# Performance work log

Measured on AMD Instinct MI355X. Metric: run time of the kernel, lower is better.

The kernel has to match this reference:

```python
import jax, jax.numpy as jnp
import numpy as np

N_NODES = 150000
N_EDGES = 2400000


def setup_inputs() -> dict:
    key = jax.random.key(0)
    ks = jax.random.split(key, 7)
    x = jax.random.normal(ks[0], (N_NODES, 9), dtype=jnp.float32)
    edge_index = jax.random.randint(ks[1], (2, N_EDGES), 0, N_NODES, dtype=jnp.int32)
    edge_weight = jax.random.uniform(ks[2], (N_EDGES,), dtype=jnp.float32, minval=0.1, maxval=1.0)
    W1 = jax.random.normal(ks[3], (9, 32), dtype=jnp.float32) * (1.0 / np.sqrt(9))
    b1 = jnp.zeros((32,), dtype=jnp.float32)
    W2 = jax.random.normal(ks[4], (32, 7), dtype=jnp.float32) * (1.0 / np.sqrt(32))
    b2 = jnp.zeros((7,), dtype=jnp.float32)
    return {"x": x, "edge_index": edge_index, "edge_weight": edge_weight,
            "W1": W1, "b1": b1, "W2": W2, "b2": b2}


def gcn_norm(edge_index, edge_weight, num_nodes):
    # PyG gcn_norm: add self-loops (weight 1), symmetric D^-1/2 A D^-1/2
    row, col = edge_index[0], edge_index[1]
    loop = jnp.arange(num_nodes, dtype=edge_index.dtype)
    row = jnp.concatenate([row, loop])
    col = jnp.concatenate([col, loop])
    w = jnp.concatenate([edge_weight, jnp.ones((num_nodes,), edge_weight.dtype)])
    deg = jax.ops.segment_sum(w, col, num_segments=num_nodes)  # [N]
    dinv = jnp.where(deg > 0, jax.lax.rsqrt(deg), 0.0)
    norm = dinv[row] * w * dinv[col]  # [E+N]
    return row, col, norm


def gcn_conv(x, W, b, row, col, norm, num_nodes):
    h = x @ W                                   # [N, out]
    msg = norm[:, None] * h[row]                # [E+N, out] gather + scale
    out = jax.ops.segment_sum(msg, col, num_segments=num_nodes)  # scatter-add
    return out + b


def reference(x, edge_index, edge_weight, W1, b1, W2, b2):
    n = x.shape[0]
    row, col, norm = gcn_norm(edge_index, edge_weight, n)
    h = jax.nn.relu(gcn_conv(x, W1, b1, row, col, norm, n))
    # dropout is identity in eval mode
    h = gcn_conv(h, W2, b2, row, col, norm, n)
    return jax.nn.log_softmax(h, axis=1)
```

## Files before the change

kernel.cpp:

```cpp
#include <hip/hip_runtime.h>
#include <hip/hip_fp16.h>

constexpr int F_IN  = 9;
constexpr int F_HID = 32;
constexpr int F_OUT = 7;

constexpr int SB_SHIFT = 13;
constexpr int SB_NODES = 1 << SB_SHIFT;
constexpr int NSB      = 19;
constexpr int SB_CAP   = 135424;
constexpr int A_EDGES  = 4096;
constexpr int FB_PER_SB= SB_NODES / 256;
constexpr int NBKT     = 586;
constexpr int NBKT_PAD = NSB * FB_PER_SB;
constexpr int BCAP     = 4864;
constexpr int B_EDGES  = 4096;
constexpr int B_CHUNKS = (SB_CAP + B_EDGES - 1) / B_EDGES;
constexpr int ROW_MASK = (1 << 18) - 1;

__device__ __forceinline__ int nt_load_int(const int* p) {
    return __builtin_nontemporal_load(p);
}

__device__ __forceinline__ unsigned pack_h2(float a, float b) {
    return (unsigned)__half_as_ushort(__float2half(a)) |
           ((unsigned)__half_as_ushort(__float2half(b)) << 16);
}
__device__ __forceinline__ float2 unpack_h2(unsigned u) {
    return make_float2(__half2float(__ushort_as_half((unsigned short)(u & 0xffffu))),
                       __half2float(__ushort_as_half((unsigned short)(u >> 16))));
}

__global__ void k_zcur(int* __restrict__ bcur) {
    int i = blockIdx.x * 256 + threadIdx.x;
    if (i < NBKT_PAD) bcur[i * 16] = i * BCAP;
}

__global__ __launch_bounds__(256) void k_histA(
    const int* __restrict__ col, int* __restrict__ ghist, int nblkA, int E)
{
    __shared__ int h[NSB];
    const int tid = threadIdx.x;
    if (tid < NSB) h[tid] = 0;
    __syncthreads();
    const int t0 = blockIdx.x * A_EDGES;
    const int kend = min(A_EDGES, E - t0);
    for (int k = tid; k < kend; k += 256)
        atomicAdd(&h[col[t0 + k] >> SB_SHIFT], 1);
    __syncthreads();
    if (tid < NSB) ghist[(size_t)tid * nblkA + blockIdx.x] = h[tid];
}

__global__ __launch_bounds__(256) void k_scanA(
    int* __restrict__ ghist, int* __restrict__ sbcnt, int nblkA)
{
    __shared__ int sc[256];
    const int s = blockIdx.x, tid = threadIdx.x;
    int* r = ghist + (size_t)s * nblkA;
    const int per = (nblkA + 255) / 256;
    const int i0 = tid * per, i1 = min(i0 + per, nblkA);

    int sum = 0;
    for (int i = i0; i < i1; ++i) sum += r[i];
    sc[tid] = sum; __syncthreads();
    for (int d = 1; d < 256; d <<= 1) {
        int u = (tid >= d) ? sc[tid - d] : 0;
        __syncthreads();
        sc[tid] += u; __syncthreads();
    }
    int run = sc[tid] - sum;
    for (int i = i0; i < i1; ++i) { int v = r[i]; r[i] = run; run += v; }
    if (tid == 255) sbcnt[s] = run;
}

__global__ __launch_bounds__(256) void k_scatA(
    const int* __restrict__ row, const int* __restrict__ col,
    const float* __restrict__ w, const int* __restrict__ ghist,
    int2* __restrict__ sbrec, int nblkA, int E)
{
    __shared__ int rb[NSB];
    __shared__ int cur[NSB];
    const int b = blockIdx.x, tid = threadIdx.x;
    if (tid < NSB) {
        rb[tid] = tid * SB_CAP + ghist[(size_t)tid * nblkA + b];
        cur[tid] = 0;
    }
    __syncthreads();
    const int t0 = b * A_EDGES;
    const int kend = min(A_EDGES, E - t0);
    for (int k = tid; k < kend; k += 256) {
        int e = t0 + k;
        int c = col[e];
        int s = c >> SB_SHIFT;
        int2 rec = make_int2(row[e] | ((c & (SB_NODES - 1)) << 18),
                             __float_as_int(w[e]));
        int rk = atomicAdd(&cur[s], 1);
        int pos = rb[s] + rk;
        if (pos < (s + 1) * SB_CAP)
            sbrec[pos] = rec;
    }
}

__global__ __launch_bounds__(256) void k_fbkt(
    const int2* __restrict__ sbrec, const int* __restrict__ sbcnt,
    int* __restrict__ bcur, int2* __restrict__ irec)
{
    __shared__ int2 s_rec[B_EDGES];
    __shared__ int hist[FB_PER_SB * 4];
    __shared__ int rbase[FB_PER_SB * 4];

    const int sb    = blockIdx.x / B_CHUNKS;
    const int chunk = blockIdx.x % B_CHUNKS;
    const int cnt   = min(sbcnt[sb], SB_CAP);
    const int k0    = chunk * B_EDGES;
    const int kend  = min(B_EDGES, cnt - k0);
    if (kend <= 0) return;

    const int tid = threadIdx.x, wv = tid >> 6;
    for (int i = tid; i < FB_PER_SB * 4; i += 256) hist[i] = 0;
    __syncthreads();

    const int base = sb * SB_CAP + k0;
    for (int k = tid; k < kend; k += 256) {
        int2 rc = sbrec[base + k];
        s_rec[k] = rc;
        int fb = ((unsigned)rc.x >> 18) >> 8;
        atomicAdd(&hist[fb * 4 + wv], 1);
    }
    __syncthreads();
    for (int i = tid; i < FB_PER_SB * 4; i += 256) {
        int c = hist[i];
        int gb = sb * FB_PER_SB + (i >> 2);
        rbase[i] = c ? atomicAdd(&bcur[gb * 16], c) : 0;
        hist[i] = 0;
    }
    __syncthreads();
    for (int k = tid; k < kend; k += 256) {
        int2 rc = s_rec[k];
        int fb = ((unsigned)rc.x >> 18) >> 8;
        int idx = fb * 4 + wv;
        int rk = atomicAdd(&hist[idx], 1);
        int pos = rbase[idx] + rk;
        int gb = sb * FB_PER_SB + fb;
        if (pos < (gb + 1) * BCAP)
            irec[pos] = rc;
    }
}

__global__ __launch_bounds__(256) void k_sortbucket(
    int2* __restrict__ irec, int* __restrict__ csr4,
    const int* __restrict__ bcur, const float* __restrict__ x,
    int4* __restrict__ meta, unsigned* __restrict__ xdh, int N)
{
    __shared__ int2  s_rec[BCAP];
    __shared__ int   hist[256];
    __shared__ float wsum[256];
    __shared__ int   nbase[256];
    __shared__ int   scur[256];

    const int b    = blockIdx.x;
    const int tid  = threadIdx.x;
    const int base = b * BCAP;
    const int cnt  = min(bcur[b * 16] - base, BCAP);

    hist[tid] = 0; wsum[tid] = 0.0f; scur[tid] = 0;
    __syncthreads();

    for (int k = tid; k < cnt; k += 256) {
        int2 rc = irec[base + k];
        s_rec[k] = rc;
        int c = ((unsigned)rc.x >> 18) & 255;
        atomicAdd(&hist[c], 1);
        atomicAdd(&wsum[c], __int_as_float(rc.y));
    }
    __syncthreads();

    int v = hist[tid];
    nbase[tid] = v;
    __syncthreads();
    for (int d = 1; d < 256; d <<= 1) {
        int u = (tid >= d) ? nbase[tid - d] : 0;
        __syncthreads();
        nbase[tid] += u;
        __syncthreads();
    }
    int excl = nbase[tid] - v;
    __syncthreads();
    nbase[tid] = excl;

    int node = b * 256 + tid;
    float dv = rsqrtf(1.0f + wsum[tid]);
    if (node < N)
        meta[node] = make_int4(base + excl, v, __float_as_int(dv), 0);
    __syncthreads();

    if (node < N) {
        float xv[F_IN];
        #pragma unroll
        for (int j = 0; j < F_IN; ++j) xv[j] = dv * x[(size_t)node * F_IN + j];
        size_t o = (size_t)node * 6;
        xdh[o + 0] = pack_h2(xv[0], xv[1]);
        xdh[o + 1] = pack_h2(xv[2], xv[3]);
        xdh[o + 2] = pack_h2(xv[4], xv[5]);
        xdh[o + 3] = pack_h2(xv[6], xv[7]);
        xdh[o + 4] = pack_h2(xv[8], 0.0f);
        xdh[o + 5] = 0u;
    }

    for (int k = tid; k < cnt; k += 256) {
        int2 rc = s_rec[k];
        int c = ((unsigned)rc.x >> 18) & 255;
        int r = atomicAdd(&scur[c], 1);
        float wf = __int_as_float(rc.y);
        int wq = min((int)(wf * 16384.0f + 0.5f), 16383);
        csr4[base + nbase[c] + r] = ((rc.x & ROW_MASK) << 14) | wq;
    }
}

__global__ __launch_bounds__(256) void k_g1mlp(
    const int* __restrict__ csr4, const int4* __restrict__ meta,
    const unsigned* __restrict__ xdh,
    const float* __restrict__ W1, const float* __restrict__ b1,
    const float* __restrict__ W2, unsigned* __restrict__ h2dh, int N)
{
    __shared__ float sW1[F_IN * F_HID];
    __shared__ float sb1[F_HID];
    __shared__ float sW2[F_HID * F_OUT];
    for (int t = threadIdx.x; t < F_IN * F_HID; t += 256) sW1[t] = W1[t];
    for (int t = threadIdx.x; t < F_HID;        t += 256) sb1[t] = b1[t];
    for (int t = threadIdx.x; t < F_HID * F_OUT; t += 256) sW2[t] = W2[t];
    __syncthreads();

    int t   = blockIdx.x * 256 + threadIdx.x;
    int i   = t >> 2;
    int sub = t & 3;
    if (i >= N) return;
    int4 m = meta[i];
    float dv = __int_as_float(m.z);

    float acc[F_IN];
    #pragma unroll
    for (int j = 0; j < F_IN; ++j) acc[j] = 0.0f;
    if (sub == 0) {
        size_t o = (size_t)i * 6;
        uint2 u01 = *reinterpret_cast<const uint2*>(xdh + o);
        uint2 u23 = *reinterpret_cast<const uint2*>(xdh + o + 2);
        unsigned u4 = xdh[o + 4];
        float2 f0 = unpack_h2(u01.x), f1 = unpack_h2(u01.y),
               f2 = unpack_h2(u23.x), f3 = unpack_h2(u23.y),
               f4 = unpack_h2(u4);
        acc[0] = f0.x; acc[1] = f0.y; acc[2] = f1.x; acc[3] = f1.y;
        acc[4] = f2.x; acc[5] = f2.y; acc[6] = f3.x; acc[7] = f3.y;
        acc[8] = f4.x;
    }
    int s = m.x, tend = m.x + m.y;
    for (int e = s + sub; e < tend; e += 4) {
        int v = nt_load_int(&csr4[e]);
        int r = (int)((unsigned)v >> 14);
        float wv = (float)(v & 16383) * (1.0f / 16384.0f);
        size_t o = (size_t)r * 6;
        uint2 u01 = *reinterpret_cast<const uint2*>(xdh + o);
        uint2 u23 = *reinterpret_cast<const uint2*>(xdh + o + 2);
        unsigned u4 = xdh[o + 4];
        float2 f0 = unpack_h2(u01.x), f1 = unpack_h2(u01.y),
               f2 = unpack_h2(u23.x), f3 = unpack_h2(u23.y),
               f4 = unpack_h2(u4);
        acc[0] = fmaf(wv, f0.x, acc[0]); acc[1] = fmaf(wv, f0.y, acc[1]);
        acc[2] = fmaf(wv, f1.x, acc[2]); acc[3] = fmaf(wv, f1.y, acc[3]);
        acc[4] = fmaf(wv, f2.x, acc[4]); acc[5] = fmaf(wv, f2.y, acc[5]);
        acc[6] = fmaf(wv, f3.x, acc[6]); acc[7] = fmaf(wv, f3.y, acc[7]);
        acc[8] = fmaf(wv, f4.x, acc[8]);
    }
    #pragma unroll
    for (int d = 1; d < 4; d <<= 1) {
        #pragma unroll
        for (int j = 0; j < F_IN; ++j)
            acc[j] += __shfl_xor(acc[j], d, 4);
    }
    #pragma unroll
    for (int j = 0; j < F_IN; ++j) acc[j] *= dv;

    float o[F_OUT];
    #pragma unroll
    for (int c = 0; c < F_OUT; ++c) o[c] = 0.0f;
    int ks = sub * 8;
    #pragma unroll
    for (int k = 0; k < 8; ++k) {
        float hk = sb1[ks + k];
        #pragma unroll
        for (int j = 0; j < F_IN; ++j) hk = fmaf(acc[j], sW1[j * F_HID + ks + k], hk);
        hk = fmaxf(hk, 0.0f);
        #pragma unroll
        for (int c = 0; c < F_OUT; ++c) o[c] = fmaf(hk, sW2[(ks + k) * F_OUT + c], o[c]);
    }
    #pragma unroll
    for (int d = 1; d < 4; d <<= 1) {
        #pragma unroll
        for (int c = 0; c < F_OUT; ++c)
            o[c] += __shfl_xor(o[c], d, 4);
    }
    float pa = dv * o[2 * sub];
    float pb = (2 * sub + 1 < F_OUT) ? dv * o[2 * sub + 1] : 0.0f;
    h2dh[(size_t)i * 4 + sub] = pack_h2(pa, pb);
}

__global__ __launch_bounds__(256) void k_g2ls(
    const int* __restrict__ csr4, const int4* __restrict__ meta,
    const unsigned* __restrict__ h2dh, const float* __restrict__ b2,
    float* __restrict__ out, int N)
{
    int t   = blockIdx.x * 256 + threadIdx.x;
    int i   = t >> 2;
    int sub = t & 3;
    if (i >= N) return;
    int4 m = meta[i];
    float dv = __int_as_float(m.z);

    float acc[F_OUT];
    #pragma unroll
    for (int c = 0; c < F_OUT; ++c) acc[c] = 0.0f;
    if (sub == 0) {
        uint4 h4 = *reinterpret_cast<const uint4*>(h2dh + (size_t)i * 4);
        float2 f0 = unpack_h2(h4.x), f1 = unpack_h2(h4.y),
               f2 = unpack_h2(h4.z), f3 = unpack_h2(h4.w);
        acc[0] = f0.x; acc[1] = f0.y; acc[2] = f1.x; acc[3] = f1.y;
        acc[4] = f2.x; acc[5] = f2.y; acc[6] = f3.x;
    }
    int s = m.x, tend = m.x + m.y;
    for (int e = s + sub; e < tend; e += 4) {
        int v = nt_load_int(&csr4[e]);
        int r = (int)((unsigned)v >> 14);
        float wv = (float)(v & 16383) * (1.0f / 16384.0f);
        uint4 h4 = *reinterpret_cast<const uint4*>(h2dh + (size_t)r * 4);
        float2 f0 = unpack_h2(h4.x), f1 = unpack_h2(h4.y),
               f2 = unpack_h2(h4.z), f3 = unpack_h2(h4.w);
        acc[0] = fmaf(wv, f0.x, acc[0]); acc[1] = fmaf(wv, f0.y, acc[1]);
        acc[2] = fmaf(wv, f1.x, acc[2]); acc[3] = fmaf(wv, f1.y, acc[3]);
        acc[4] = fmaf(wv, f2.x, acc[4]); acc[5] = fmaf(wv, f2.y, acc[5]);
        acc[6] = fmaf(wv, f3.x, acc[6]);
    }
    #pragma unroll
    for (int d = 1; d < 4; d <<= 1) {
        #pragma unroll
        for (int c = 0; c < F_OUT; ++c)
            acc[c] += __shfl_xor(acc[c], d, 4);
    }

    float vv[F_OUT];
    float mx = -1e30f;
    #pragma unroll
    for (int c = 0; c < F_OUT; ++c) {
        vv[c] = dv * acc[c] + b2[c];
        mx = fmaxf(mx, vv[c]);
    }
    float ss = 0.0f;
    #pragma unroll
    for (int c = 0; c < F_OUT; ++c) ss += __expf(vv[c] - mx);
    float ls = __logf(ss);
    for (int c = sub; c < F_OUT; c += 4)
        out[(size_t)i * F_OUT + c] = vv[c] - mx - ls;
}

extern "C" void kernel_launch(void* const* d_in, const int* in_sizes, int n_in,
                              void* d_out, int out_size, void* d_ws, size_t ws_size,
                              hipStream_t stream) {
    const float* x  = (const float*)d_in[0];
    const int*   ei = (const int*)  d_in[1];
    const float* ew = (const float*)d_in[2];
    const float* W1 = (const float*)d_in[3];
    const float* b1 = (const float*)d_in[4];
    const float* W2 = (const float*)d_in[5];
    const float* b2 = (const float*)d_in[6];
    float* out = (float*)d_out;

    const int N = in_sizes[0] / F_IN;
    const int E = in_sizes[2];
    const int* row = ei;
    const int* col = ei + E;
    const int nblkA = (E + A_EDGES - 1) / A_EDGES;

    int2* sbrec = (int2*)d_ws;
    int2* irec  = sbrec + (size_t)NSB * SB_CAP;
    int*  csr4  = (int*)irec;
    int*  bcur  = (int*)(irec + (size_t)NBKT * BCAP);
    int*  ghist = bcur + (size_t)NBKT_PAD * 16;
    int*  sbcnt = ghist + (size_t)NSB * nblkA;
    int4*     meta = (int4*)d_ws;
    unsigned* xdh  = (unsigned*)(meta + N);
    unsigned* h2dh = xdh + (size_t)N * 6;

    const int gB = NSB * B_CHUNKS;
    const int gN4 = (4 * N + 255) / 256;

    k_zcur      <<<(NBKT_PAD + 255) / 256, 256, 0, stream>>>(bcur);
    k_histA     <<<nblkA, 256, 0, stream>>>(col, ghist, nblkA, E);
    k_scanA     <<<NSB, 256, 0, stream>>>(ghist, sbcnt, nblkA);
    k_scatA     <<<nblkA, 256, 0, stream>>>(row, col, ew, ghist, sbrec, nblkA, E);
    k_fbkt      <<<gB, 256, 0, stream>>>(sbrec, sbcnt, bcur, irec);
    k_sortbucket<<<NBKT, 256, 0, stream>>>(irec, csr4, bcur, x, meta, xdh, N);
    k_g1mlp     <<<gN4, 256, 0, stream>>>(csr4, meta, xdh, W1, b1, W2, h2dh, N);
    k_g2ls      <<<gN4, 256, 0, stream>>>(csr4, meta, h2dh, b2, out, N);
}
```

Measured before the change: 139.9 us.

## Replace two-level superbucket sort with single-pass 586-bucket counting scatter

The edge bucketing pipeline is collapsed from a two-level radix sort (19 superbuckets, then fine buckets via global atomics) into one counting sort over 586 fine buckets, with a per-chunk histogram, a per-bucket column scan and a direct scatter. This removes a kernel launch, the intermediate superbucket buffer pass, and the global atomic cursors. Weights are quantized during the scatter, so the sort kernel only reorders packed words. The scan now reads a strided, column-major histogram, and the scatter writes to 586 destinations per chunk, which may make those writes less coalesced.

```diff
diff --git a/kernel.cpp b/kernel.cpp
--- a/kernel.cpp
+++ b/kernel.cpp
@@ -5,23 +5,13 @@
 constexpr int F_HID = 32;
 constexpr int F_OUT = 7;
 
-constexpr int SB_SHIFT = 13;
-constexpr int SB_NODES = 1 << SB_SHIFT;
-constexpr int NSB      = 19;
-constexpr int SB_CAP   = 135424;
-constexpr int A_EDGES  = 4096;
-constexpr int FB_PER_SB= SB_NODES / 256;
-constexpr int NBKT     = 586;
-constexpr int NBKT_PAD = NSB * FB_PER_SB;
-constexpr int BCAP     = 4864;
-constexpr int B_EDGES  = 4096;
-constexpr int B_CHUNKS = (SB_CAP + B_EDGES - 1) / B_EDGES;
-constexpr int ROW_MASK = (1 << 18) - 1;
+constexpr int NBKT   = 586;
+constexpr int BCAP   = 4864;
+constexpr int CHUNK  = 4096;
 
 __device__ __forceinline__ int nt_load_int(const int* p) {
     return __builtin_nontemporal_load(p);
 }
-
 __device__ __forceinline__ unsigned pack_h2(float a, float b) {
     return (unsigned)__half_as_ushort(__float2half(a)) |
            ((unsigned)__half_as_ushort(__float2half(b)) << 16);
@@ -31,37 +21,32 @@
                        __half2float(__ushort_as_half((unsigned short)(u >> 16))));
 }
 
-__global__ void k_zcur(int* __restrict__ bcur) {
-    int i = blockIdx.x * 256 + threadIdx.x;
-    if (i < NBKT_PAD) bcur[i * 16] = i * BCAP;
-}
-
-__global__ __launch_bounds__(256) void k_histA(
-    const int* __restrict__ col, int* __restrict__ ghist, int nblkA, int E)
-{
-    __shared__ int h[NSB];
+__global__ __launch_bounds__(256) void k_hist(
+    const int* __restrict__ col, int* __restrict__ ghist, int E)
+{
+    __shared__ int h[NBKT];
     const int tid = threadIdx.x;
-    if (tid < NSB) h[tid] = 0;
-    __syncthreads();
-    const int t0 = blockIdx.x * A_EDGES;
-    const int kend = min(A_EDGES, E - t0);
+    for (int i = tid; i < NBKT; i += 256) h[i] = 0;
+    __syncthreads();
+    const int t0 = blockIdx.x * CHUNK;
+    const int kend = min(CHUNK, E - t0);
     for (int k = tid; k < kend; k += 256)
-        atomicAdd(&h[col[t0 + k] >> SB_SHIFT], 1);
-    __syncthreads();
-    if (tid < NSB) ghist[(size_t)tid * nblkA + blockIdx.x] = h[tid];
-}
-
-__global__ __launch_bounds__(256) void k_scanA(
-    int* __restrict__ ghist, int* __restrict__ sbcnt, int nblkA)
+        atomicAdd(&h[col[t0 + k] >> 8], 1);
+    __syncthreads();
+    int* g = ghist + (size_t)blockIdx.x * NBKT;
+    for (int i = tid; i < NBKT; i += 256) g[i] = h[i];
+}
+
+__global__ __launch_bounds__(256) void k_scan(
+    int* __restrict__ ghist, int* __restrict__ cnt, int nchunk)
 {
     __shared__ int sc[256];
-    const int s = blockIdx.x, tid = threadIdx.x;
-    int* r = ghist + (size_t)s * nblkA;
-    const int per = (nblkA + 255) / 256;
-    const int i0 = tid * per, i1 = min(i0 + per, nblkA);
+    const int b = blockIdx.x, tid = threadIdx.x;
+    const int per = (nchunk + 255) / 256;
+    const int i0 = tid * per, i1 = min(i0 + per, nchunk);
 
     int sum = 0;
-    for (int i = i0; i < i1; ++i) sum += r[i];
+    for (int i = i0; i < i1; ++i) sum += ghist[(size_t)i * NBKT + b];
     sc[tid] = sum; __syncthreads();
     for (int d = 1; d < 256; d <<= 1) {
         int u = (tid >= d) ? sc[tid - d] : 0;
@@ -69,90 +54,46 @@
         sc[tid] += u; __syncthreads();
     }
     int run = sc[tid] - sum;
-    for (int i = i0; i < i1; ++i) { int v = r[i]; r[i] = run; run += v; }
-    if (tid == 255) sbcnt[s] = run;
-}
-
-__global__ __launch_bounds__(256) void k_scatA(
+    for (int i = i0; i < i1; ++i) {
+        int v = ghist[(size_t)i * NBKT + b];
+        ghist[(size_t)i * NBKT + b] = run;
+        run += v;
+    }
+    if (tid == 255) cnt[b] = run;
+}
+
+__global__ __launch_bounds__(256) void k_scat(
     const int* __restrict__ row, const int* __restrict__ col,
     const float* __restrict__ w, const int* __restrict__ ghist,
-    int2* __restrict__ sbrec, int nblkA, int E)
-{
-    __shared__ int rb[NSB];
-    __shared__ int cur[NSB];
-    const int b = blockIdx.x, tid = threadIdx.x;
-    if (tid < NSB) {
-        rb[tid] = tid * SB_CAP + ghist[(size_t)tid * nblkA + b];
-        cur[tid] = 0;
-    }
-    __syncthreads();
-    const int t0 = b * A_EDGES;
-    const int kend = min(A_EDGES, E - t0);
+    int2* __restrict__ irec, int E)
+{
+    __shared__ int sbase[NBKT];
+    __shared__ int scur[NBKT];
+    const int tid = threadIdx.x;
+    const int* g = ghist + (size_t)blockIdx.x * NBKT;
+    for (int i = tid; i < NBKT; i += 256) { sbase[i] = g[i]; scur[i] = 0; }
+    __syncthreads();
+    const int t0 = blockIdx.x * CHUNK;
+    const int kend = min(CHUNK, E - t0);
     for (int k = tid; k < kend; k += 256) {
         int e = t0 + k;
         int c = col[e];
-        int s = c >> SB_SHIFT;
-        int2 rec = make_int2(row[e] | ((c & (SB_NODES - 1)) << 18),
-                             __float_as_int(w[e]));
-        int rk = atomicAdd(&cur[s], 1);
-        int pos = rb[s] + rk;
-        if (pos < (s + 1) * SB_CAP)
-            sbrec[pos] = rec;
-    }
-}
-
-__global__ __launch_bounds__(256) void k_fbkt(
-    const int2* __restrict__ sbrec, const int* __restrict__ sbcnt,
-    int* __restrict__ bcur, int2* __restrict__ irec)
-{
-    __shared__ int2 s_rec[B_EDGES];
-    __shared__ int hist[FB_PER_SB * 4];
-    __shared__ int rbase[FB_PER_SB * 4];
-
-    const int sb    = blockIdx.x / B_CHUNKS;
-    const int chunk = blockIdx.x % B_CHUNKS;
-    const int cnt   = min(sbcnt[sb], SB_CAP);
-    const int k0    = chunk * B_EDGES;
-    const int kend  = min(B_EDGES, cnt - k0);
-    if (kend <= 0) return;
-
-    const int tid = threadIdx.x, wv = tid >> 6;
-    for (int i = tid; i < FB_PER_SB * 4; i += 256) hist[i] = 0;
-    __syncthreads();
-
-    const int base = sb * SB_CAP + k0;
-    for (int k = tid; k < kend; k += 256) {
-        int2 rc = sbrec[base + k];
-        s_rec[k] = rc;
-        int fb = ((unsigned)rc.x >> 18) >> 8;
-        atomicAdd(&hist[fb * 4 + wv], 1);
-    }
-    __syncthreads();
-    for (int i = tid; i < FB_PER_SB * 4; i += 256) {
-        int c = hist[i];
-        int gb = sb * FB_PER_SB + (i >> 2);
-        rbase[i] = c ? atomicAdd(&bcur[gb * 16], c) : 0;
-        hist[i] = 0;
-    }
-    __syncthreads();
-    for (int k = tid; k < kend; k += 256) {
-        int2 rc = s_rec[k];
-        int fb = ((unsigned)rc.x >> 18) >> 8;
-        int idx = fb * 4 + wv;
-        int rk = atomicAdd(&hist[idx], 1);
-        int pos = rbase[idx] + rk;
-        int gb = sb * FB_PER_SB + fb;
-        if (pos < (gb + 1) * BCAP)
-            irec[pos] = rc;
+        int b = c >> 8;
+        int wq = min((int)(w[e] * 16384.0f + 0.5f), 16383);
+        int rk = atomicAdd(&scur[b], 1);
+        int pos = b * BCAP + sbase[b] + rk;
+        if (pos < (b + 1) * BCAP)
+            irec[pos] = make_int2((row[e] << 14) | wq, c & 255);
     }
 }
 
 __global__ __launch_bounds__(256) void k_sortbucket(
-    int2* __restrict__ irec, int* __restrict__ csr4,
-    const int* __restrict__ bcur, const float* __restrict__ x,
+    const int2* __restrict__ irec, int* __restrict__ csr4,
+    const int* __restrict__ cnt, const float* __restrict__ x,
     int4* __restrict__ meta, unsigned* __restrict__ xdh, int N)
 {
-    __shared__ int2  s_rec[BCAP];
+    __shared__ int           srw[BCAP];
+    __shared__ unsigned char scb[BCAP];
     __shared__ int   hist[256];
     __shared__ float wsum[256];
     __shared__ int   nbase[256];
@@ -161,17 +102,18 @@
     const int b    = blockIdx.x;
     const int tid  = threadIdx.x;
     const int base = b * BCAP;
-    const int cnt  = min(bcur[b * 16] - base, BCAP);
+    const int c_n  = min(cnt[b], BCAP);
 
     hist[tid] = 0; wsum[tid] = 0.0f; scur[tid] = 0;
     __syncthreads();
 
-    for (int k = tid; k < cnt; k += 256) {
+    for (int k = tid; k < c_n; k += 256) {
         int2 rc = irec[base + k];
-        s_rec[k] = rc;
-        int c = ((unsigned)rc.x >> 18) & 255;
+        srw[k] = rc.x;
+        unsigned char c = (unsigned char)(rc.y & 255);
+        scb[k] = c;
         atomicAdd(&hist[c], 1);
-        atomicAdd(&wsum[c], __int_as_float(rc.y));
+        atomicAdd(&wsum[c], (float)(rc.x & 16383) * (1.0f / 16384.0f));
     }
     __syncthreads();
 
@@ -190,11 +132,8 @@
 
     int node = b * 256 + tid;
     float dv = rsqrtf(1.0f + wsum[tid]);
-    if (node < N)
+    if (node < N) {
         meta[node] = make_int4(base + excl, v, __float_as_int(dv), 0);
-    __syncthreads();
-
-    if (node < N) {
         float xv[F_IN];
         #pragma unroll
         for (int j = 0; j < F_IN; ++j) xv[j] = dv * x[(size_t)node * F_IN + j];
@@ -206,14 +145,13 @@
         xdh[o + 4] = pack_h2(xv[8], 0.0f);
         xdh[o + 5] = 0u;
     }
-
-    for (int k = tid; k < cnt; k += 256) {
-        int2 rc = s_rec[k];
-        int c = ((unsigned)rc.x >> 18) & 255;
+    __syncthreads();
+
+    for (int k = tid; k < c_n; k += 256) {
+        int rw = srw[k];
+        unsigned char c = scb[k];
         int r = atomicAdd(&scur[c], 1);
-        float wf = __int_as_float(rc.y);
-        int wq = min((int)(wf * 16384.0f + 0.5f), 16383);
-        csr4[base + nbase[c] + r] = ((rc.x & ROW_MASK) << 14) | wq;
+        csr4[base + nbase[c] + r] = rw;
     }
 }
 
@@ -280,9 +218,9 @@
     #pragma unroll
     for (int j = 0; j < F_IN; ++j) acc[j] *= dv;
 
-    float o[F_OUT];
-    #pragma unroll
-    for (int c = 0; c < F_OUT; ++c) o[c] = 0.0f;
+    float o7[F_OUT];
+    #pragma unroll
+    for (int c = 0; c < F_OUT; ++c) o7[c] = 0.0f;
     int ks = sub * 8;
     #pragma unroll
     for (int k = 0; k < 8; ++k) {
@@ -291,16 +229,16 @@
         for (int j = 0; j < F_IN; ++j) hk = fmaf(acc[j], sW1[j * F_HID + ks + k], hk);
         hk = fmaxf(hk, 0.0f);
         #pragma unroll
-        for (int c = 0; c < F_OUT; ++c) o[c] = fmaf(hk, sW2[(ks + k) * F_OUT + c], o[c]);
+        for (int c = 0; c < F_OUT; ++c) o7[c] = fmaf(hk, sW2[(ks + k) * F_OUT + c], o7[c]);
     }
     #pragma unroll
     for (int d = 1; d < 4; d <<= 1) {
         #pragma unroll
         for (int c = 0; c < F_OUT; ++c)
-            o[c] += __shfl_xor(o[c], d, 4);
-    }
-    float pa = dv * o[2 * sub];
-    float pb = (2 * sub + 1 < F_OUT) ? dv * o[2 * sub + 1] : 0.0f;
+            o7[c] += __shfl_xor(o7[c], d, 4);
+    }
+    float pa = dv * o7[2 * sub];
+    float pb = (2 * sub + 1 < F_OUT) ? dv * o7[2 * sub + 1] : 0.0f;
     h2dh[(size_t)i * 4 + sub] = pack_h2(pa, pb);
 }
 
@@ -377,27 +315,23 @@
     const int E = in_sizes[2];
     const int* row = ei;
     const int* col = ei + E;
-    const int nblkA = (E + A_EDGES - 1) / A_EDGES;
-
-    int2* sbrec = (int2*)d_ws;
-    int2* irec  = sbrec + (size_t)NSB * SB_CAP;
-    int*  csr4  = (int*)irec;
-    int*  bcur  = (int*)(irec + (size_t)NBKT * BCAP);
-    int*  ghist = bcur + (size_t)NBKT_PAD * 16;
-    int*  sbcnt = ghist + (size_t)NSB * nblkA;
-    int4*     meta = (int4*)d_ws;
-    unsigned* xdh  = (unsigned*)(meta + N);
-    unsigned* h2dh = xdh + (size_t)N * 6;
-
-    const int gB = NSB * B_CHUNKS;
+    const int nchunk = (E + CHUNK - 1) / CHUNK;
+
+    char* p = (char*)d_ws;
+    int2*     irec  = (int2*)p;      p += sizeof(int2) * (size_t)NBKT * BCAP;
+    int*      csr4  = (int*)p;       p += sizeof(int)  * (size_t)NBKT * BCAP;
+    int4*     meta  = (int4*)p;      p += sizeof(int4) * (size_t)N;
+    unsigned* xdh   = (unsigned*)p;  p += sizeof(unsigned) * (size_t)N * 6;
+    unsigned* h2dh  = (unsigned*)p;  p += sizeof(unsigned) * (size_t)N * 4;
+    int*      ghist = (int*)p;       p += sizeof(int) * (size_t)nchunk * NBKT;
+    int*      cnt   = (int*)p;       p += sizeof(int) * NBKT;
+
     const int gN4 = (4 * N + 255) / 256;
 
-    k_zcur      <<<(NBKT_PAD + 255) / 256, 256, 0, stream>>>(bcur);
-    k_histA     <<<nblkA, 256, 0, stream>>>(col, ghist, nblkA, E);
-    k_scanA     <<<NSB, 256, 0, stream>>>(ghist, sbcnt, nblkA);
-    k_scatA     <<<nblkA, 256, 0, stream>>>(row, col, ew, ghist, sbrec, nblkA, E);
-    k_fbkt      <<<gB, 256, 0, stream>>>(sbrec, sbcnt, bcur, irec);
-    k_sortbucket<<<NBKT, 256, 0, stream>>>(irec, csr4, bcur, x, meta, xdh, N);
+    k_hist      <<<nchunk, 256, 0, stream>>>(col, ghist, E);
+    k_scan      <<<NBKT, 256, 0, stream>>>(ghist, cnt, nchunk);
+    k_scat      <<<nchunk, 256, 0, stream>>>(row, col, ew, ghist, irec, E);
+    k_sortbucket<<<NBKT, 256, 0, stream>>>(irec, csr4, cnt, x, meta, xdh, N);
     k_g1mlp     <<<gN4, 256, 0, stream>>>(csr4, meta, xdh, W1, b1, W2, h2dh, N);
     k_g2ls      <<<gN4, 256, 0, stream>>>(csr4, meta, h2dh, b2, out, N);
 }
```

Measured after the change: 134.3 us. 4.0% less time.
